# Performance work log

Hardware: AMD Instinct MI355X
Metric: run time of the kernel (lower is better)

## Reference

```python
import jax, jax.numpy as jnp
import numpy as np

N = 100000
E = 800000
D_IN = 128
D_HID = 128
D_EMB = 128
D_OUT = 2


def setup_inputs() -> dict:
    key = jax.random.key(0)
    ks = jax.random.split(key, 16)
    x = jax.random.normal(ks[0], (N, D_IN), dtype=jnp.float32)
    edge_index = jax.random.randint(ks[1], (2, E), 0, N, dtype=jnp.int64)

    def lin(k, d_out, d_in, scale):
        return jax.random.normal(k, (d_out, d_in), dtype=jnp.float32) * scale

    s1 = 1.0 / np.sqrt(D_IN)
    s2 = 1.0 / np.sqrt(D_HID)
    s3 = 1.0 / np.sqrt(D_EMB)
    return {
        "x": x,
        "edge_index": edge_index,
        # layer 1: in -> hidden  (lin_l has bias, lin_r no bias, as in PyG SAGEConv)
        "Wl1": lin(ks[2], D_HID, D_IN, s1), "bl1": jnp.zeros((D_HID,), jnp.float32),
        "Wr1": lin(ks[3], D_HID, D_IN, s1),
        # layer 2: hidden -> hidden
        "Wl2": lin(ks[4], D_HID, D_HID, s2), "bl2": jnp.zeros((D_HID,), jnp.float32),
        "Wr2": lin(ks[5], D_HID, D_HID, s2),
        # layer 3: hidden -> embedding
        "Wl3": lin(ks[6], D_EMB, D_HID, s2), "bl3": jnp.zeros((D_EMB,), jnp.float32),
        "Wr3": lin(ks[7], D_EMB, D_HID, s2),
        # output head: embedding -> output (bias)
        "Wo": lin(ks[8], D_OUT, D_EMB, s3), "bo": jnp.zeros((D_OUT,), jnp.float32),
    }


def _sage_conv(x, src, dst, Wl, bl, Wr):
    # mean-aggregate neighbor (source) features onto destination nodes
    msg = x[src]                                             # [E, d]
    agg = jax.ops.segment_sum(msg, dst, num_segments=N)      # [N, d]
    deg = jax.ops.segment_sum(jnp.ones((src.shape[0],), x.dtype), dst, num_segments=N)
    agg = agg / jnp.maximum(deg, 1.0)[:, None]
    # out = lin_l(agg) + lin_r(x)
    return agg @ Wl.T + bl + x @ Wr.T


def reference(x, edge_index, Wl1, bl1, Wr1, Wl2, bl2, Wr2, Wl3, bl3, Wr3, Wo, bo):
    src, dst = edge_index[0], edge_index[1]
    h = jax.nn.relu(_sage_conv(x, src, dst, Wl1, bl1, Wr1))   # dropout is identity in eval
    h = jax.nn.relu(_sage_conv(h, src, dst, Wl2, bl2, Wr2))
    h = _sage_conv(h, src, dst, Wl3, bl3, Wr3)                # no relu on last conv
    return h @ Wo.T + bo                                      # [N, D_OUT]
```

## Files before the change

kernel.cpp:

```cpp
#include <hip/hip_runtime.h>
#include <stdint.h>

typedef unsigned int u32;
typedef unsigned short u16;
typedef __bf16 bf16x8 __attribute__((ext_vector_type(8)));
typedef float floatx16 __attribute__((ext_vector_type(16)));
typedef u32 u32x4 __attribute__((ext_vector_type(4)));
typedef float floatx4 __attribute__((ext_vector_type(4)));

__device__ __forceinline__ u16 f2b(float f) {
    u32 u = __builtin_bit_cast(u32, f);
    u32 r = u + 0x7FFFu + ((u >> 16) & 1u);
    return (u16)(r >> 16);
}
__device__ __forceinline__ float lo2f(u32 u) { return __builtin_bit_cast(float, u << 16); }
__device__ __forceinline__ float hi2f(u32 u) { return __builtin_bit_cast(float, u & 0xFFFF0000u); }


__global__ void detect_kernel(const int* __restrict__ ei, const u32* __restrict__ xw,
                              int* __restrict__ flags, int* __restrict__ ghist) {
    int t = threadIdx.x;
    ghist[t] = 0;
    if (t < 64) {
        int v = ei[2 * t + 1];
        unsigned long long b1 = __ballot(v == 0);
        u32 w = xw[t];
        u32 e = (w >> 7) & 0xFF;
        int plaus = (e == 0) || (e >= 90 && e <= 140);
        unsigned long long b2 = __ballot(plaus);
        if (t == 0) {
            flags[0] = (b1 == ~0ULL) ? 1 : 0;
            flags[1] = (b2 == ~0ULL) ? 1 : 0;
        }
    }
}

__device__ __forceinline__ int load_id(const int* __restrict__ ei, int is64, size_t pos, int N) {
    int v = is64 ? ei[2 * pos] : ei[pos];
    unsigned u = (unsigned)v;
    if (u >= (unsigned)N) u = 0;
    return (int)u;
}

__device__ __forceinline__ float load_f(const void* __restrict__ p, int isbf, size_t i) {
    if (isbf) {
        u16 s = ((const u16*)p)[i];
        return __builtin_bit_cast(float, ((u32)s) << 16);
    }
    return ((const float*)p)[i];
}


__global__ void convert_x_kernel(const void* __restrict__ xraw, const int* __restrict__ flags,
                                 u32* __restrict__ xb, int count4) {
    int i = blockIdx.x * 256 + threadIdx.x;
    if (i >= count4) return;
    if (flags[1]) {
        ((u32x4*)xb)[i] = ((const u32x4*)xraw)[i];
    } else {
        const floatx4* f4 = (const floatx4*)xraw;
        floatx4 f0 = f4[2 * i], f1 = f4[2 * i + 1];
        u32x4 o;
        o.x = (u32)f2b(f0.x) | ((u32)f2b(f0.y) << 16);
        o.y = (u32)f2b(f0.z) | ((u32)f2b(f0.w) << 16);
        o.z = (u32)f2b(f1.x) | ((u32)f2b(f1.y) << 16);
        o.w = (u32)f2b(f1.z) | ((u32)f2b(f1.w) << 16);
        ((u32x4*)xb)[i] = o;
    }
}

__global__ void convert_smalls_kernel(const void* b0, const void* b1, const void* b2,
                                      const void* Wo, const void* bo,
                                      const int* __restrict__ flags, float* __restrict__ out) {
    int t = threadIdx.x;
    int isbf = flags[1];
    if (t < 128) out[t] = load_f(b0, isbf, t);
    else if (t < 256) out[t] = load_f(b1, isbf, t - 128);
    else if (t < 384) out[t] = load_f(b2, isbf, t - 256);
    else if (t < 640) out[t] = load_f(Wo, isbf, t - 384);
    else if (t < 642) out[t] = load_f(bo, isbf, t - 640);
}


__global__ void bucket_hist_kernel(const int* __restrict__ ei, int E,
                                   const int* __restrict__ flags, int N,
                                   int* __restrict__ ghist) {
    __shared__ int lh[1024];
    int t = threadIdx.x;
    for (int i = t; i < 1024; i += 256) lh[i] = 0;
    __syncthreads();
    int is64 = flags[0];
    for (int e = blockIdx.x * 256 + t; e < E; e += gridDim.x * 256) {
        int d = load_id(ei, is64, (size_t)E + e, N);
        atomicAdd(&lh[d >> 8], 1);
    }
    __syncthreads();
    for (int i = t; i < 1024; i += 256)
        if (lh[i]) atomicAdd(&ghist[i], lh[i]);
}

__global__ void bucket_scan_kernel(const int* __restrict__ ghist, int* __restrict__ bbase,
                                   int* __restrict__ gcur) {
    __shared__ int wsum[16];
    int t = threadIdx.x;
    int lane = t & 63, wid = t >> 6;
    int v = ghist[t];
    int inc = v;
#pragma unroll
    for (int off = 1; off < 64; off <<= 1) {
        int o = __shfl_up(inc, off);
        if (lane >= off) inc += o;
    }
    if (lane == 63) wsum[wid] = inc;
    __syncthreads();
    int wpre = 0;
    for (int w = 0; w < wid; ++w) wpre += wsum[w];
    int excl = wpre + inc - v;
    bbase[t] = excl;
    gcur[t] = excl;
}

#define CH 4096

__global__ void bucket_scatter_kernel(const int* __restrict__ ei, int E,
                                      const int* __restrict__ flags, int N,
                                      int* __restrict__ gcur, u32* __restrict__ csrbkt) {
    __shared__ int lhist[1024], loff[1024], lcur[1024], gbase[1024], wsum[16];
    __shared__ u32 ebuf[CH];
    __shared__ u16 ebkt[CH];
    int t = threadIdx.x;
    int cbase = blockIdx.x * CH;
    int cn = E - cbase;
    if (cn > CH) cn = CH;
    lhist[t] = 0;
    __syncthreads();
    int is64 = flags[0];
    int mysrc[4], myb[4], mydl[4];
#pragma unroll
    for (int k = 0; k < 4; ++k) {
        int i = t + k * 1024;
        myb[k] = -1;
        if (i < cn) {
            int e = cbase + i;
            int s = load_id(ei, is64, (size_t)e, N);
            int d = load_id(ei, is64, (size_t)E + e, N);
            mysrc[k] = s;
            mydl[k] = d & 255;
            myb[k] = d >> 8;
            atomicAdd(&lhist[myb[k]], 1);
        }
    }
    __syncthreads();
    int lane = t & 63, wid = t >> 6;
    int v = lhist[t];
    int inc = v;
#pragma unroll
    for (int off = 1; off < 64; off <<= 1) {
        int o = __shfl_up(inc, off);
        if (lane >= off) inc += o;
    }
    if (lane == 63) wsum[wid] = inc;
    __syncthreads();
    int wpre = 0;
    for (int w = 0; w < wid; ++w) wpre += wsum[w];
    int excl = wpre + inc - v;
    loff[t] = excl;
    lcur[t] = excl;
    if (v > 0) gbase[t] = atomicAdd(&gcur[t], v);
    __syncthreads();
#pragma unroll
    for (int k = 0; k < 4; ++k) {
        if (myb[k] >= 0) {
            int pos = atomicAdd(&lcur[myb[k]], 1);
            ebuf[pos] = (u32)mysrc[k] | ((u32)mydl[k] << 24);
            ebkt[pos] = (u16)myb[k];
        }
    }
    __syncthreads();
#pragma unroll
    for (int k = 0; k < 4; ++k) {
        int i = t + k * 1024;
        if (i < cn) {
            int bb = ebkt[i];
            csrbkt[gbase[bb] + (i - loff[bb])] = ebuf[i];
        }
    }
}

#define CAP3 8192

__global__ void csr_build_kernel(const u32* __restrict__ csrbkt, const int* __restrict__ ghist,
                                 const int* __restrict__ bbase, int N,
                                 int* __restrict__ offs, int* __restrict__ cnt,
                                 float* __restrict__ invd, int* __restrict__ csr) {
    __shared__ int lh[256], lo[256], lcur[256], wsum[4];
    __shared__ u32 sbuf[CAP3];
    int t = threadIdx.x;
    int b = blockIdx.x;
    int base = bbase[b];
    int cb = ghist[b];
    int d0 = b << 8;
    lh[t] = 0;
    __syncthreads();
    for (int i = t; i < cb; i += 256) atomicAdd(&lh[csrbkt[base + i] >> 24], 1);
    __syncthreads();
    int lane = t & 63, wid = t >> 6;
    int v = lh[t];
    int inc = v;
#pragma unroll
    for (int off = 1; off < 64; off <<= 1) {
        int o = __shfl_up(inc, off);
        if (lane >= off) inc += o;
    }
    if (lane == 63) wsum[wid] = inc;
    __syncthreads();
    int wpre = 0;
    for (int w = 0; w < wid; ++w) wpre += wsum[w];
    int excl = wpre + inc - v;
    lo[t] = excl;
    lcur[t] = excl;
    int d = d0 + t;
    if (d < N) {
        offs[d] = base + excl;
        cnt[d] = v;
        invd[d] = 1.0f / (float)(v > 1 ? v : 1);
    }
    __syncthreads();
    if (cb <= CAP3) {
        for (int i = t; i < cb; i += 256) {
            u32 e = csrbkt[base + i];
            int pos = atomicAdd(&lcur[e >> 24], 1);
            sbuf[pos] = e & 0xFFFFFFu;
        }
        __syncthreads();
        for (int i = t; i < cb; i += 256) csr[base + i] = (int)sbuf[i];
    } else {
        int c = base + lo[t];
        for (int i = 0; i < cb; ++i) {
            u32 e = csrbkt[base + i];
            if ((int)(e >> 24) == t) csr[c++] = (int)(e & 0xFFFFFFu);
        }
    }
}


__global__ void wprep_kernel(const void* __restrict__ Wl, const void* __restrict__ Wr,
                             const int* __restrict__ flags, u16* __restrict__ Wcp) {
    int t = blockIdx.x * 256 + threadIdx.x;
    int isbf = flags[1];
    int lane = t & 63;
    int jt = (t >> 6) & 3;
    int s = t >> 8;
    int n = lane & 31;
    int q = lane >> 5;
    int j = jt * 32 + n;
#pragma unroll
    for (int jj = 0; jj < 8; ++jj) {
        int k = s * 16 + q * 8 + jj;
        float v = (k < 128) ? load_f(Wl, isbf, (size_t)j * 128 + k)
                            : load_f(Wr, isbf, (size_t)j * 128 + (k - 128));
        Wcp[t * 8 + jj] = f2b(v);
    }
}


__global__ void agg_kernel(const u32* __restrict__ F2, const int* __restrict__ offsets,
                           const int* __restrict__ cnt, const float* __restrict__ inv_deg,
                           const int* __restrict__ csr, u32* __restrict__ Aout, int N) {
    int nd = (blockIdx.x * 256 + threadIdx.x) >> 6;
    int lane = threadIdx.x & 63;
    if (nd >= N) return;
    int start = offsets[nd];
    int num = cnt[nd];
    float a0 = 0.f, a1 = 0.f;
    int i = 0;
    for (; i + 8 <= num; i += 8) {
        int s0 = csr[start + i + 0], s1 = csr[start + i + 1];
        int s2 = csr[start + i + 2], s3 = csr[start + i + 3];
        int s4 = csr[start + i + 4], s5 = csr[start + i + 5];
        int s6 = csr[start + i + 6], s7 = csr[start + i + 7];
        u32 u0 = F2[(size_t)s0 * 64 + lane];
        u32 u1 = F2[(size_t)s1 * 64 + lane];
        u32 u2 = F2[(size_t)s2 * 64 + lane];
        u32 u3 = F2[(size_t)s3 * 64 + lane];
        u32 u4 = F2[(size_t)s4 * 64 + lane];
        u32 u5 = F2[(size_t)s5 * 64 + lane];
        u32 u6 = F2[(size_t)s6 * 64 + lane];
        u32 u7 = F2[(size_t)s7 * 64 + lane];
        a0 += lo2f(u0) + lo2f(u1) + lo2f(u2) + lo2f(u3) +
              lo2f(u4) + lo2f(u5) + lo2f(u6) + lo2f(u7);
        a1 += hi2f(u0) + hi2f(u1) + hi2f(u2) + hi2f(u3) +
              hi2f(u4) + hi2f(u5) + hi2f(u6) + hi2f(u7);
    }
    for (; i + 4 <= num; i += 4) {
        int s0 = csr[start + i + 0], s1 = csr[start + i + 1];
        int s2 = csr[start + i + 2], s3 = csr[start + i + 3];
        u32 u0 = F2[(size_t)s0 * 64 + lane];
        u32 u1 = F2[(size_t)s1 * 64 + lane];
        u32 u2 = F2[(size_t)s2 * 64 + lane];
        u32 u3 = F2[(size_t)s3 * 64 + lane];
        a0 += lo2f(u0) + lo2f(u1) + lo2f(u2) + lo2f(u3);
        a1 += hi2f(u0) + hi2f(u1) + hi2f(u2) + hi2f(u3);
    }
    for (; i < num; ++i) {
        u32 u = F2[(size_t)csr[start + i] * 64 + lane];
        a0 += lo2f(u);
        a1 += hi2f(u);
    }
    float sc = inv_deg[nd];
    a0 *= sc;
    a1 *= sc;
    Aout[(size_t)nd * 64 + lane] = (u32)f2b(a0) | ((u32)f2b(a1) << 16);
}


__global__ void gemm_kernel(const u32* __restrict__ aggb, u32* Fio,
                            const u16* __restrict__ Wcp, const float* __restrict__ biasf,
                            int N, int relu, const float* __restrict__ headw,
                            const int* __restrict__ flags, void* __restrict__ outp) {
    int tid = threadIdx.x;
    int w = tid >> 6;
    int lane = tid & 63;
    int nbase = blockIdx.x * 128;
    int n = lane & 31;
    int q = lane >> 5;
    int rowl = w * 32 + n;
    int node = nbase + rowl;
    int nodeC = (node < N) ? node : (N - 1);
    const u32* aRow = aggb + (size_t)nodeC * 64 + q * 4;
    const u32* fRow = Fio + (size_t)nodeC * 64 + q * 4;

    floatx16 acc0 = 0.0f, acc1 = 0.0f, acc2 = 0.0f, acc3 = 0.0f;

#pragma unroll
    for (int s = 0; s < 16; ++s) {
        const u32* ap = (s < 8) ? (aRow + (size_t)s * 8) : (fRow + (size_t)(s - 8) * 8);
        bf16x8 a = *reinterpret_cast<const bf16x8*>(ap);
        const u16* bp = Wcp + (size_t)((s * 4) * 64 + lane) * 8;
        bf16x8 b0 = *reinterpret_cast<const bf16x8*>(bp);
        bf16x8 b1 = *reinterpret_cast<const bf16x8*>(bp + 64 * 8);
        bf16x8 b2 = *reinterpret_cast<const bf16x8*>(bp + 2 * 64 * 8);
        bf16x8 b3 = *reinterpret_cast<const bf16x8*>(bp + 3 * 64 * 8);
        acc0 = __builtin_amdgcn_mfma_f32_32x32x16_bf16(a, b0, acc0, 0, 0, 0);
        acc1 = __builtin_amdgcn_mfma_f32_32x32x16_bf16(a, b1, acc1, 0, 0, 0);
        acc2 = __builtin_amdgcn_mfma_f32_32x32x16_bf16(a, b2, acc2, 0, 0, 0);
        acc3 = __builtin_amdgcn_mfma_f32_32x32x16_bf16(a, b3, acc3, 0, 0, 0);
    }

    int mbase = nbase + w * 32;
    floatx16 accs[4] = {acc0, acc1, acc2, acc3};

    if (outp == nullptr) {
#pragma unroll
        for (int jt = 0; jt < 4; ++jt) {
            int j0 = jt * 32 + n;
            float bf = biasf[j0];
#pragma unroll
            for (int r = 0; r < 16; ++r) {
                int row = (r & 3) + 8 * (r >> 2) + 4 * q;
                int nodeS = mbase + row;
                if (nodeS < N) {
                    float v = accs[jt][r] + bf;
                    if (relu) v = fmaxf(v, 0.0f);
                    u16* dst16 = (u16*)&Fio[(size_t)nodeS * 64];
                    dst16[j0] = f2b(v);
                }
            }
        }
    } else {
        int isbf = flags[1];
#pragma unroll
        for (int r = 0; r < 16; ++r) {
            float p0 = 0.f, p1 = 0.f;
#pragma unroll
            for (int jt = 0; jt < 4; ++jt) {
                int j = jt * 32 + n;
                float v = accs[jt][r] + biasf[j];
                p0 += v * headw[j];
                p1 += v * headw[128 + j];
            }
#pragma unroll
            for (int off = 16; off > 0; off >>= 1) {
                p0 += __shfl_xor(p0, off);
                p1 += __shfl_xor(p1, off);
            }
            if (n == 0) {
                int row = (r & 3) + 8 * (r >> 2) + 4 * q;
                int nodeS = mbase + row;
                if (nodeS < N) {
                    float o0 = p0 + headw[256];
                    float o1 = p1 + headw[257];
                    if (isbf)
                        ((u32*)outp)[nodeS] = (u32)f2b(o0) | ((u32)f2b(o1) << 16);
                    else
                        ((float2*)outp)[nodeS] = make_float2(o0, o1);
                }
            }
        }
    }
}

extern "C" void kernel_launch(void* const* d_in, const int* in_sizes, int n_in,
                              void* d_out, int out_size, void* d_ws, size_t ws_size,
                              hipStream_t stream) {
    const int N = in_sizes[0] / 128;
    const int E = in_sizes[1] / 2;

    const void* x = d_in[0];
    const int* ei = (const int*)d_in[1];
    const void* Wl[3] = {d_in[2], d_in[5], d_in[8]};
    const void* bl[3] = {d_in[3], d_in[6], d_in[9]};
    const void* Wr[3] = {d_in[4], d_in[7], d_in[10]};
    const void* Wo = d_in[11];
    const void* bo = d_in[12];

    char* p = (char*)d_ws;
    auto alloc = [&](size_t bytes) -> char* {
        char* r = p;
        p += (bytes + 255) & ~(size_t)255;
        return r;
    };
    int* flags = (int*)alloc(256);
    int* cnt = (int*)alloc((size_t)N * 4);
    int* offs = (int*)alloc((size_t)N * 4);
    float* invd = (float*)alloc((size_t)N * 4);
    float* smalls = (float*)alloc(642 * 4);
    int* ghist = (int*)alloc(1024 * 4);
    int* bbase = (int*)alloc(1024 * 4);
    int* gcur = (int*)alloc(1024 * 4);
    int* csr = (int*)alloc((size_t)E * 4);
    u16* Wcp = (u16*)alloc((size_t)3 * 4096 * 8 * 2);
    u32* xb = (u32*)alloc((size_t)N * 64 * 4);
    u32* aggb = (u32*)alloc((size_t)N * 64 * 4);
    u32* csrbkt = aggb;
    (void)ws_size;

    const int NB = (N + 255) / 256;
    const int wb = (N + 3) / 4;
    const int gb = (N + 127) / 128;
    const int cb = (N * 16 + 255) / 256;
    const int sb = (E + CH - 1) / CH;

    detect_kernel<<<1, 1024, 0, stream>>>(ei, (const u32*)x, flags, ghist);
    bucket_hist_kernel<<<256, 256, 0, stream>>>(ei, E, flags, N, ghist);
    bucket_scan_kernel<<<1, 1024, 0, stream>>>(ghist, bbase, gcur);
    bucket_scatter_kernel<<<sb, 1024, 0, stream>>>(ei, E, flags, N, gcur, csrbkt);
    csr_build_kernel<<<NB, 256, 0, stream>>>(csrbkt, ghist, bbase, N, offs, cnt, invd, csr);

    convert_x_kernel<<<cb, 256, 0, stream>>>(x, flags, xb, N * 16);
    convert_smalls_kernel<<<1, 768, 0, stream>>>(bl[0], bl[1], bl[2], Wo, bo, flags, smalls);
    for (int l = 0; l < 3; ++l)
        wprep_kernel<<<16, 256, 0, stream>>>(Wl[l], Wr[l], flags, Wcp + (size_t)l * 32768);

    agg_kernel<<<wb, 256, 0, stream>>>(xb, offs, cnt, invd, csr, aggb, N);
    gemm_kernel<<<gb, 256, 0, stream>>>(aggb, xb, Wcp, smalls, N, 1, nullptr, flags, nullptr);
    agg_kernel<<<wb, 256, 0, stream>>>(xb, offs, cnt, invd, csr, aggb, N);
    gemm_kernel<<<gb, 256, 0, stream>>>(aggb, xb, Wcp + 32768, smalls + 128, N, 1, nullptr, flags, nullptr);
    agg_kernel<<<wb, 256, 0, stream>>>(xb, offs, cnt, invd, csr, aggb, N);
    gemm_kernel<<<gb, 256, 0, stream>>>(aggb, xb, Wcp + 65536, smalls + 256, N, 0,
                                        smalls + 384, flags, d_out);
}
```

Baseline: 371.2 us.

## Merge weight/bias prep kernels, drop cnt/invd arrays, process four nodes per wave

The three wprep launches and the convert_smalls launch become one prep_kernel, which removes launch overhead. The CSR now stores N+1 offsets, so degree and inverse degree are computed inline, and the separate cnt and invd arrays and their loads go away. Each wavefront in agg_kernel now aggregates four consecutive nodes in sequence instead of one, with a quarter of the launched blocks. The sequential node loop may lower memory-level parallelism in the latency-bound gather.

```diff
diff --git a/kernel.cpp b/kernel.cpp
--- a/kernel.cpp
+++ b/kernel.cpp
@@ -69,18 +69,6 @@
     }
 }
 
-__global__ void convert_smalls_kernel(const void* b0, const void* b1, const void* b2,
-                                      const void* Wo, const void* bo,
-                                      const int* __restrict__ flags, float* __restrict__ out) {
-    int t = threadIdx.x;
-    int isbf = flags[1];
-    if (t < 128) out[t] = load_f(b0, isbf, t);
-    else if (t < 256) out[t] = load_f(b1, isbf, t - 128);
-    else if (t < 384) out[t] = load_f(b2, isbf, t - 256);
-    else if (t < 640) out[t] = load_f(Wo, isbf, t - 384);
-    else if (t < 642) out[t] = load_f(bo, isbf, t - 640);
-}
-
 
 __global__ void bucket_hist_kernel(const int* __restrict__ ei, int E,
                                    const int* __restrict__ flags, int N,
@@ -190,9 +178,8 @@
 #define CAP3 8192
 
 __global__ void csr_build_kernel(const u32* __restrict__ csrbkt, const int* __restrict__ ghist,
-                                 const int* __restrict__ bbase, int N,
-                                 int* __restrict__ offs, int* __restrict__ cnt,
-                                 float* __restrict__ invd, int* __restrict__ csr) {
+                                 const int* __restrict__ bbase, int N, int E,
+                                 int* __restrict__ offs, int* __restrict__ csr) {
     __shared__ int lh[256], lo[256], lcur[256], wsum[4];
     __shared__ u32 sbuf[CAP3];
     int t = threadIdx.x;
@@ -201,6 +188,7 @@
     int cb = ghist[b];
     int d0 = b << 8;
     lh[t] = 0;
+    if (b == 0 && t == 0) offs[N] = E;
     __syncthreads();
     for (int i = t; i < cb; i += 256) atomicAdd(&lh[csrbkt[base + i] >> 24], 1);
     __syncthreads();
@@ -220,11 +208,7 @@
     lo[t] = excl;
     lcur[t] = excl;
     int d = d0 + t;
-    if (d < N) {
-        offs[d] = base + excl;
-        cnt[d] = v;
-        invd[d] = 1.0f / (float)(v > 1 ? v : 1);
-    }
+    if (d < N) offs[d] = base + excl;
     __syncthreads();
     if (cb <= CAP3) {
         for (int i = t; i < cb; i += 256) {
@@ -244,73 +228,96 @@
 }
 
 
-__global__ void wprep_kernel(const void* __restrict__ Wl, const void* __restrict__ Wr,
-                             const int* __restrict__ flags, u16* __restrict__ Wcp) {
-    int t = blockIdx.x * 256 + threadIdx.x;
+__global__ void prep_kernel(const void* Wl1, const void* Wr1, const void* Wl2, const void* Wr2,
+                            const void* Wl3, const void* Wr3, const void* b1, const void* b2,
+                            const void* b3, const void* Wo, const void* bo,
+                            const int* __restrict__ flags, u16* __restrict__ Wcp,
+                            float* __restrict__ smalls) {
     int isbf = flags[1];
-    int lane = t & 63;
-    int jt = (t >> 6) & 3;
-    int s = t >> 8;
-    int n = lane & 31;
-    int q = lane >> 5;
-    int j = jt * 32 + n;
-#pragma unroll
-    for (int jj = 0; jj < 8; ++jj) {
-        int k = s * 16 + q * 8 + jj;
-        float v = (k < 128) ? load_f(Wl, isbf, (size_t)j * 128 + k)
-                            : load_f(Wr, isbf, (size_t)j * 128 + (k - 128));
-        Wcp[t * 8 + jj] = f2b(v);
-    }
-}
-
-
-__global__ void agg_kernel(const u32* __restrict__ F2, const int* __restrict__ offsets,
-                           const int* __restrict__ cnt, const float* __restrict__ inv_deg,
+    int blk = blockIdx.x;
+    if (blk < 48) {
+        int l = blk >> 4;
+        const void* Wl = (l == 0) ? Wl1 : (l == 1) ? Wl2 : Wl3;
+        const void* Wr = (l == 0) ? Wr1 : (l == 1) ? Wr2 : Wr3;
+        u16* Wout = Wcp + (size_t)l * 32768;
+        int t = (blk & 15) * 256 + threadIdx.x;
+        int lane = t & 63;
+        int jt = (t >> 6) & 3;
+        int s = t >> 8;
+        int n = lane & 31;
+        int q = lane >> 5;
+        int j = jt * 32 + n;
+#pragma unroll
+        for (int jj = 0; jj < 8; ++jj) {
+            int k = s * 16 + q * 8 + jj;
+            float v = (k < 128) ? load_f(Wl, isbf, (size_t)j * 128 + k)
+                                : load_f(Wr, isbf, (size_t)j * 128 + (k - 128));
+            Wout[t * 8 + jj] = f2b(v);
+        }
+    } else {
+        for (int t = threadIdx.x; t < 642; t += 256) {
+            float v;
+            if (t < 128) v = load_f(b1, isbf, t);
+            else if (t < 256) v = load_f(b2, isbf, t - 128);
+            else if (t < 384) v = load_f(b3, isbf, t - 256);
+            else if (t < 640) v = load_f(Wo, isbf, t - 384);
+            else v = load_f(bo, isbf, t - 640);
+            smalls[t] = v;
+        }
+    }
+}
+
+
+__global__ void agg_kernel(const u32* __restrict__ F2, const int* __restrict__ offs,
                            const int* __restrict__ csr, u32* __restrict__ Aout, int N) {
-    int nd = (blockIdx.x * 256 + threadIdx.x) >> 6;
+    int gw = (blockIdx.x * 256 + threadIdx.x) >> 6;
     int lane = threadIdx.x & 63;
-    if (nd >= N) return;
-    int start = offsets[nd];
-    int num = cnt[nd];
-    float a0 = 0.f, a1 = 0.f;
-    int i = 0;
-    for (; i + 8 <= num; i += 8) {
-        int s0 = csr[start + i + 0], s1 = csr[start + i + 1];
-        int s2 = csr[start + i + 2], s3 = csr[start + i + 3];
-        int s4 = csr[start + i + 4], s5 = csr[start + i + 5];
-        int s6 = csr[start + i + 6], s7 = csr[start + i + 7];
-        u32 u0 = F2[(size_t)s0 * 64 + lane];
-        u32 u1 = F2[(size_t)s1 * 64 + lane];
-        u32 u2 = F2[(size_t)s2 * 64 + lane];
-        u32 u3 = F2[(size_t)s3 * 64 + lane];
-        u32 u4 = F2[(size_t)s4 * 64 + lane];
-        u32 u5 = F2[(size_t)s5 * 64 + lane];
-        u32 u6 = F2[(size_t)s6 * 64 + lane];
-        u32 u7 = F2[(size_t)s7 * 64 + lane];
-        a0 += lo2f(u0) + lo2f(u1) + lo2f(u2) + lo2f(u3) +
-              lo2f(u4) + lo2f(u5) + lo2f(u6) + lo2f(u7);
-        a1 += hi2f(u0) + hi2f(u1) + hi2f(u2) + hi2f(u3) +
-              hi2f(u4) + hi2f(u5) + hi2f(u6) + hi2f(u7);
-    }
-    for (; i + 4 <= num; i += 4) {
-        int s0 = csr[start + i + 0], s1 = csr[start + i + 1];
-        int s2 = csr[start + i + 2], s3 = csr[start + i + 3];
-        u32 u0 = F2[(size_t)s0 * 64 + lane];
-        u32 u1 = F2[(size_t)s1 * 64 + lane];
-        u32 u2 = F2[(size_t)s2 * 64 + lane];
-        u32 u3 = F2[(size_t)s3 * 64 + lane];
-        a0 += lo2f(u0) + lo2f(u1) + lo2f(u2) + lo2f(u3);
-        a1 += hi2f(u0) + hi2f(u1) + hi2f(u2) + hi2f(u3);
-    }
-    for (; i < num; ++i) {
-        u32 u = F2[(size_t)csr[start + i] * 64 + lane];
-        a0 += lo2f(u);
-        a1 += hi2f(u);
-    }
-    float sc = inv_deg[nd];
-    a0 *= sc;
-    a1 *= sc;
-    Aout[(size_t)nd * 64 + lane] = (u32)f2b(a0) | ((u32)f2b(a1) << 16);
+    int nd0 = gw * 4;
+    if (nd0 >= N) return;
+    int nd1 = nd0 + 4 < N ? nd0 + 4 : N;
+    for (int nd = nd0; nd < nd1; ++nd) {
+        int start = offs[nd];
+        int num = offs[nd + 1] - start;
+        float a0 = 0.f, a1 = 0.f;
+        int i = 0;
+        for (; i + 8 <= num; i += 8) {
+            int s0 = csr[start + i + 0], s1 = csr[start + i + 1];
+            int s2 = csr[start + i + 2], s3 = csr[start + i + 3];
+            int s4 = csr[start + i + 4], s5 = csr[start + i + 5];
+            int s6 = csr[start + i + 6], s7 = csr[start + i + 7];
+            u32 u0 = F2[(size_t)s0 * 64 + lane];
+            u32 u1 = F2[(size_t)s1 * 64 + lane];
+            u32 u2 = F2[(size_t)s2 * 64 + lane];
+            u32 u3 = F2[(size_t)s3 * 64 + lane];
+            u32 u4 = F2[(size_t)s4 * 64 + lane];
+            u32 u5 = F2[(size_t)s5 * 64 + lane];
+            u32 u6 = F2[(size_t)s6 * 64 + lane];
+            u32 u7 = F2[(size_t)s7 * 64 + lane];
+            a0 += lo2f(u0) + lo2f(u1) + lo2f(u2) + lo2f(u3) +
+                  lo2f(u4) + lo2f(u5) + lo2f(u6) + lo2f(u7);
+            a1 += hi2f(u0) + hi2f(u1) + hi2f(u2) + hi2f(u3) +
+                  hi2f(u4) + hi2f(u5) + hi2f(u6) + hi2f(u7);
+        }
+        for (; i + 4 <= num; i += 4) {
+            int s0 = csr[start + i + 0], s1 = csr[start + i + 1];
+            int s2 = csr[start + i + 2], s3 = csr[start + i + 3];
+            u32 u0 = F2[(size_t)s0 * 64 + lane];
+            u32 u1 = F2[(size_t)s1 * 64 + lane];
+            u32 u2 = F2[(size_t)s2 * 64 + lane];
+            u32 u3 = F2[(size_t)s3 * 64 + lane];
+            a0 += lo2f(u0) + lo2f(u1) + lo2f(u2) + lo2f(u3);
+            a1 += hi2f(u0) + hi2f(u1) + hi2f(u2) + hi2f(u3);
+        }
+        for (; i < num; ++i) {
+            u32 u = F2[(size_t)csr[start + i] * 64 + lane];
+            a0 += lo2f(u);
+            a1 += hi2f(u);
+        }
+        float sc = 1.0f / (float)(num > 1 ? num : 1);
+        a0 *= sc;
+        a1 *= sc;
+        Aout[(size_t)nd * 64 + lane] = (u32)f2b(a0) | ((u32)f2b(a1) << 16);
+    }
 }
 
 
@@ -421,9 +428,7 @@
         return r;
     };
     int* flags = (int*)alloc(256);
-    int* cnt = (int*)alloc((size_t)N * 4);
-    int* offs = (int*)alloc((size_t)N * 4);
-    float* invd = (float*)alloc((size_t)N * 4);
+    int* offs = (int*)alloc(((size_t)N + 1) * 4);
     float* smalls = (float*)alloc(642 * 4);
     int* ghist = (int*)alloc(1024 * 4);
     int* bbase = (int*)alloc(1024 * 4);
@@ -436,27 +441,26 @@
     (void)ws_size;
 
     const int NB = (N + 255) / 256;
-    const int wb = (N + 3) / 4;
     const int gb = (N + 127) / 128;
     const int cb = (N * 16 + 255) / 256;
     const int sb = (E + CH - 1) / CH;
+    const int ab = ((N + 3) / 4 + 3) / 4;
 
     detect_kernel<<<1, 1024, 0, stream>>>(ei, (const u32*)x, flags, ghist);
     bucket_hist_kernel<<<256, 256, 0, stream>>>(ei, E, flags, N, ghist);
     bucket_scan_kernel<<<1, 1024, 0, stream>>>(ghist, bbase, gcur);
     bucket_scatter_kernel<<<sb, 1024, 0, stream>>>(ei, E, flags, N, gcur, csrbkt);
-    csr_build_kernel<<<NB, 256, 0, stream>>>(csrbkt, ghist, bbase, N, offs, cnt, invd, csr);
+    csr_build_kernel<<<NB, 256, 0, stream>>>(csrbkt, ghist, bbase, N, E, offs, csr);
 
     convert_x_kernel<<<cb, 256, 0, stream>>>(x, flags, xb, N * 16);
-    convert_smalls_kernel<<<1, 768, 0, stream>>>(bl[0], bl[1], bl[2], Wo, bo, flags, smalls);
-    for (int l = 0; l < 3; ++l)
-        wprep_kernel<<<16, 256, 0, stream>>>(Wl[l], Wr[l], flags, Wcp + (size_t)l * 32768);
-
-    agg_kernel<<<wb, 256, 0, stream>>>(xb, offs, cnt, invd, csr, aggb, N);
+    prep_kernel<<<49, 256, 0, stream>>>(Wl[0], Wr[0], Wl[1], Wr[1], Wl[2], Wr[2],
+                                        bl[0], bl[1], bl[2], Wo, bo, flags, Wcp, smalls);
+
+    agg_kernel<<<ab, 256, 0, stream>>>(xb, offs, csr, aggb, N);
     gemm_kernel<<<gb, 256, 0, stream>>>(aggb, xb, Wcp, smalls, N, 1, nullptr, flags, nullptr);
-    agg_kernel<<<wb, 256, 0, stream>>>(xb, offs, cnt, invd, csr, aggb, N);
+    agg_kernel<<<ab, 256, 0, stream>>>(xb, offs, csr, aggb, N);
     gemm_kernel<<<gb, 256, 0, stream>>>(aggb, xb, Wcp + 32768, smalls + 128, N, 1, nullptr, flags, nullptr);
-    agg_kernel<<<wb, 256, 0, stream>>>(xb, offs, cnt, invd, csr, aggb, N);
+    agg_kernel<<<ab, 256, 0, stream>>>(xb, offs, csr, aggb, N);
     gemm_kernel<<<gb, 256, 0, stream>>>(aggb, xb, Wcp + 65536, smalls + 256, N, 0,
                                         smalls + 384, flags, d_out);
 }
```

Result: faster. 350.5 us (-5.6%).
